# Performance work log

Hardware: AMD Instinct MI355X
Metric: run time of the kernel (lower is better)

## Reference

```python
import jax, jax.numpy as jnp
import numpy as np

B, S, H, IN, OUT, T = 1024, 256, 128, 2, 2, 512


def setup_inputs() -> dict:
    key = jax.random.key(0)
    ks = jax.random.split(key, 7)
    scale = 1.0 / np.sqrt(H)  # PyTorch LSTM init range ~ U(-1/sqrt(H), 1/sqrt(H))
    return {
        "x": jax.random.normal(ks[0], (B, S, IN), jnp.float32),
        "w_ih": jax.random.normal(ks[1], (4 * H, IN), jnp.float32) * scale,
        "w_hh": jax.random.normal(ks[2], (4 * H, H), jnp.float32) * scale,
        "b_ih": jax.random.normal(ks[3], (4 * H,), jnp.float32) * scale,
        "b_hh": jax.random.normal(ks[4], (4 * H,), jnp.float32) * scale,
        "w_fc": jax.random.normal(ks[5], (OUT, H), jnp.float32) * scale,
        "b_fc": jax.random.normal(ks[6], (OUT,), jnp.float32) * scale,
        "target_length": T,
    }


def reference(x, w_ih, w_hh, b_ih, b_hh, w_fc, b_fc, target_length):
    # PyTorch nn.LSTM cell, gate order (i, f, g, o). Dropout is identity (eval mode).
    bias = b_ih + b_hh
    hdim = w_hh.shape[1]

    def cell(h, c, x_t):
        gates = x_t @ w_ih.T + h @ w_hh.T + bias  # [B, 4H]
        i, f, g, o = jnp.split(gates, 4, axis=-1)
        c_new = jax.nn.sigmoid(f) * c + jax.nn.sigmoid(i) * jnp.tanh(g)
        h_new = jax.nn.sigmoid(o) * jnp.tanh(c_new)
        return h_new, c_new

    bsz = x.shape[0]
    h0 = jnp.zeros((bsz, hdim), x.dtype)
    c0 = jnp.zeros((bsz, hdim), x.dtype)

    # Encode input sequence
    def enc_step(carry, x_t):
        h, c = carry
        h, c = cell(h, c, x_t)
        return (h, c), None

    (h, c), _ = jax.lax.scan(enc_step, (h0, c0), jnp.swapaxes(x, 0, 1))

    inp0 = x[:, -1, :]  # [B, 2]

    def dec_step(carry, _):
        h, c, inp = carry
        h, c = cell(h, c, inp)
        pred = h @ w_fc.T + b_fc  # [B, 2]
        return (h, c, pred), pred

    _, preds = jax.lax.scan(dec_step, (h, c, inp0), None, length=target_length)
    return jnp.swapaxes(preds, 0, 1)  # [B, target_length, 2]
```

## Files before the change

### kernel.cpp

```cpp
#include <hip/hip_runtime.h>

typedef unsigned short ush;
typedef unsigned int uint32;
typedef __attribute__((ext_vector_type(8))) __bf16 bf16x8;
typedef __attribute__((ext_vector_type(4))) float f32x4;
typedef __attribute__((ext_vector_type(4))) int i32x4;
typedef __attribute__((ext_vector_type(16))) char c8x16;

#define NBLK 256
#define RB   4
#define NTHR 512
#define SENC 256
#define TDEC 512
#define HDIM 128
#define HSTR 144
#define H8STR 144
#define XSTR 520
#define PSTR 1024
#define HIST_USH_PER_BLK (TDEC * RB * HDIM)
#define WS_NEEDED ((size_t)NBLK * HIST_USH_PER_BLK * 2)

#define LOG2E  1.4426950408889634f
#define LOG2E2 2.8853900817779268f

__device__ __forceinline__ float bf2f(ush u){
  uint32 v = ((uint32)u) << 16;
  return __builtin_bit_cast(float, v);
}
__device__ __forceinline__ ush f2bf(float f){
  return __builtin_bit_cast(ush, (__bf16)f);
}
__device__ __forceinline__ float lo16f(uint32 w){ return __builtin_bit_cast(float, w << 16); }
__device__ __forceinline__ float hi16f(uint32 w){ return __builtin_bit_cast(float, w & 0xFFFF0000u); }

__device__ __forceinline__ float loadf(const void* p, int i, bool f32){
  return f32 ? ((const float*)p)[i] : bf2f(((const ush*)p)[i]);
}
__device__ __forceinline__ f32x4 M1(bf16x8 a, bf16x8 b, f32x4 c){
  return __builtin_amdgcn_mfma_f32_16x16x32_bf16(a, b, c, 0, 0, 0);
}
__device__ __forceinline__ i32x4 MI(i32x4 a, i32x4 b, i32x4 c){
  return __builtin_amdgcn_mfma_i32_16x16x64_i8(a, b, c, 0, 0, 0);
}

template<bool DEFER>
__global__ void __launch_bounds__(NTHR, 2)
lstm_kernel(const void* __restrict__ xg,  const void* __restrict__ wih,
            const void* __restrict__ whh, const void* __restrict__ bih,
            const void* __restrict__ bhh, const void* __restrict__ wfc,
            const void* __restrict__ bfc, void* __restrict__ outg,
            void* __restrict__ ws)
{
  __shared__ __attribute__((aligned(16))) ush x_lds[RB * XSTR];
  __shared__ __attribute__((aligned(16))) ush h_lds[2][RB * HSTR];
  __shared__ __attribute__((aligned(16))) char h8s[2][RB * H8STR];
  __shared__ __attribute__((aligned(16))) ush pred_lds[RB][PSTR];
  __shared__ __attribute__((aligned(16))) float ppart[2][RB][2][4];

  constexpr bool DF = DEFER;

  const int tid   = threadIdx.x;
  const int lane  = tid & 63;
  const int wv    = tid >> 6;
  const int n     = lane & 15;
  const int q     = lane >> 4;
  const int q8    = q * 8;
  const int q16   = q * 16;
  const int gbase = wv << 4;
  const int blk   = blockIdx.x;

  const uint32* wp = (const uint32*)whh;
  int cnt = 0;
  #pragma unroll
  for (int i = 0; i < 64; ++i){
    uint32 e = (wp[i] >> 7) & 0xFFu;
    cnt += (e >= 90u && e <= 140u) ? 1 : 0;
  }
  const bool isf32 = (cnt < 40);

  for (int i = tid; i < 2 * RB * HSTR; i += NTHR) h_lds[0][i] = 0;
  for (int i = tid; i < 2 * RB * H8STR; i += NTHR) ((char*)h8s)[i] = 0;

  if (!isf32){
    if (tid < 256){
      int row = tid >> 6, c = (tid & 63) * 8;
      uint4 v = *reinterpret_cast<const uint4*>((const ush*)xg + (blk * RB + row) * (SENC * 2) + c);
      *reinterpret_cast<uint4*>(&x_lds[row * XSTR + c]) = v;
    }
  } else {
    for (int i = tid; i < RB * SENC * 2; i += NTHR){
      int row = i >> 9, c = i & 511;
      x_lds[row * XSTR + c] = f2bf(((const float*)xg)[(blk * RB + row) * (SENC * 2) + c]);
    }
  }

  float wih0v[4], wih1v[4], biasv[4], smulv[4];
  i32x4 ifr[4][2];
  #pragma unroll
  for (int p = 0; p < 4; ++p){
    int g = p * 128 + gbase + n;
    biasv[p] = loadf(bih, g, isf32) + loadf(bhh, g, isf32);
    wih0v[p] = loadf(wih, g * 2 + 0, isf32);
    wih1v[p] = loadf(wih, g * 2 + 1, isf32);
    float w[2][16]; float m = 0.0f;
    #pragma unroll
    for (int kh = 0; kh < 2; ++kh){
      #pragma unroll
      for (int j = 0; j < 16; ++j){
        float v = loadf(whh, g * HDIM + kh * 64 + q16 + j, isf32);
        w[kh][j] = v; m = __builtin_fmaxf(m, __builtin_fabsf(v));
      }
    }
    m = __builtin_fmaxf(m, __shfl_xor(m, 16, 64));
    m = __builtin_fmaxf(m, __shfl_xor(m, 32, 64));
    m = __builtin_fmaxf(m, 1e-20f);
    float sinv = 127.0f / m;
    smulv[p] = m * (1.0f / (127.0f * 127.0f));
    #pragma unroll
    for (int kh = 0; kh < 2; ++kh){
      c8x16 c;
      #pragma unroll
      for (int j = 0; j < 16; ++j)
        c[j] = (char)(int)__builtin_rintf(w[kh][j] * sinv);
      ifr[p][kh] = __builtin_bit_cast(i32x4, c);
    }
  }
  const bool ispred = (wv == 0) || (wv == 3) || (wv == 5) || (wv == 6);
  const bool issum  = (wv == 1);
  const int  pkk    = (wv == 0) ? 0 : (wv == 3) ? 1 : (wv == 5) ? 2 : 3;
  const int  pofs   = pkk * 32 + q8;
  bf16x8 wpfr;
  #pragma unroll
  for (int j = 0; j < 8; ++j)
    wpfr[j] = (__bf16)loadf(wfc, (n & 1) * HDIM + pkk * 32 + q8 + j, isf32);
  f32x4 predC;
  {
    float pb = (wv == 0) ? loadf(bfc, n & 1, isf32) : 0.0f;
    predC[0] = pb; predC[1] = pb; predC[2] = pb; predC[3] = pb;
  }

  float cc = 0.0f;
  const int arow   = (n >> 2) * HSTR;
  const int a8row  = (n >> 2) * H8STR;
  const int hwofs  = q * HSTR + gbase + n;
  const int h8wofs = q * H8STR + gbase + n;
  const f32x4 Z  = {0.0f, 0.0f, 0.0f, 0.0f};
  const i32x4 IZ = {0, 0, 0, 0};

  ush* hlane = (ush*)ws + (((size_t)blk) << 18) + q * HDIM + gbase + n;

  __syncthreads();

#define LOADA8(RBUF) \
    const char* ha = &h8s[RBUF][a8row]; \
    i32x4 a80 = *reinterpret_cast<const i32x4*>(ha + q16); \
    i32x4 a81 = *reinterpret_cast<const i32x4*>(ha + 64 + q16);

#define GATEMM8 \
    i32x4 G2 = MI(a80, ifr[2][0], IZ); \
    i32x4 G0 = MI(a80, ifr[0][0], IZ); \
    i32x4 G1 = MI(a80, ifr[1][0], IZ); \
    i32x4 G3 = MI(a80, ifr[3][0], IZ); \
    G2 = MI(a81, ifr[2][1], G2); \
    G0 = MI(a81, ifr[0][1], G0); \
    G1 = MI(a81, ifr[1][1], G1); \
    G3 = MI(a81, ifr[3][1], G3);

#define TAIL8(WBUF, DOHIST, HS, BX0, BX1, BX2, BX3) \
    float g2 = __builtin_fmaf((float)G2[0], smulv[2], BX2); \
    float Eg = __builtin_amdgcn_exp2f(g2 * LOG2E2); \
    float g0 = __builtin_fmaf((float)G0[0], smulv[0], BX0); \
    float ei = __builtin_amdgcn_exp2f(-g0 * LOG2E); \
    float g1 = __builtin_fmaf((float)G1[0], smulv[1], BX1); \
    float ef = __builtin_amdgcn_exp2f(-g1 * LOG2E); \
    float g3 = __builtin_fmaf((float)G3[0], smulv[3], BX3); \
    float eo = __builtin_amdgcn_exp2f(-g3 * LOG2E); \
    float sitg = (Eg - 1.0f) * __builtin_amdgcn_rcpf((1.0f + ei) * (Eg + 1.0f)); \
    float sf = __builtin_amdgcn_rcpf(1.0f + ef); \
    cc = sf * cc + sitg; \
    float ccl = __builtin_amdgcn_fmed3f(cc, -20.0f, 20.0f); \
    float Ec = __builtin_amdgcn_exp2f(ccl * LOG2E2); \
    float hh = (Ec - 1.0f) * __builtin_amdgcn_rcpf((1.0f + eo) * (Ec + 1.0f)); \
    h8s[WBUF][h8wofs] = (char)(int)__builtin_rintf(hh * 127.0f); \
    if constexpr (DF){ if (DOHIST) hlane[(HS) * 512] = f2bf(hh); } \
    else { h_lds[WBUF][hwofs] = f2bf(hh); }

#define ENCSTEP(RBUF, WBUF, T, DOHIST, HS) { \
    LOADA8(RBUF) \
    uint32 xw = *reinterpret_cast<const uint32*>(&x_lds[q * XSTR + (T) * 2]); \
    GATEMM8 \
     \
    float xa = lo16f(xw), xb = hi16f(xw); \
    float bx0 = biasv[0] + __builtin_fmaf(wih0v[0], xa, wih1v[0] * xb); \
    float bx1 = biasv[1] + __builtin_fmaf(wih0v[1], xa, wih1v[1] * xb); \
    float bx2 = biasv[2] + __builtin_fmaf(wih0v[2], xa, wih1v[2] * xb); \
    float bx3 = biasv[3] + __builtin_fmaf(wih0v[3], xa, wih1v[3] * xb); \
    TAIL8(WBUF, DOHIST, HS, bx0, bx1, bx2, bx3) \
    __syncthreads(); \
  }

#define DECSTEP(RBUF, WBUF, D) { \
    LOADA8(RBUF) \
    if constexpr (!DF) { \
      bf16x8 pfrag; \
      if (ispred) pfrag = *reinterpret_cast<const bf16x8*>(&h_lds[RBUF][arow] + pofs); \
      f32x4 pp; \
      if (issum && (D) > 0 && n < 2) \
        pp = *reinterpret_cast<const f32x4*>(&ppart[((D) - 1) & 1][q][n][0]); \
      GATEMM8 \
      f32x4 PP; \
      if (ispred) PP = M1(pfrag, wpfr, predC); \
      if (issum && (D) > 0 && n < 2) \
        pred_lds[q][((D) - 1) * 2 + n] = f2bf(pp[0] + pp[1] + pp[2] + pp[3]); \
      if (ispred && n < 2) ppart[(D) & 1][q][n][pkk] = PP[0]; \
      TAIL8(WBUF, 0, 0, biasv[0], biasv[1], biasv[2], biasv[3]) \
    } else { \
      GATEMM8 \
      TAIL8(WBUF, 1, (D) + 1, biasv[0], biasv[1], biasv[2], biasv[3]) \
    } \
    __syncthreads(); \
  }

  #pragma unroll 1
  for (int s = 0; s < SENC; s += 2){
    ENCSTEP(0, 1, s, 0, 0)
    ENCSTEP(1, 0, s + 1, 0, 0)
  }
  ENCSTEP(0, 1, SENC - 1, 1, 0)

  {
    float bfc0 = loadf(bfc, 0, isf32), bfc1 = loadf(bfc, 1, isf32);
    #pragma unroll
    for (int p = 0; p < 4; ++p){
      int g = p * 128 + gbase + n;
      biasv[p] = biasv[p] + wih0v[p] * bfc0 + wih1v[p] * bfc1;
      float w[2][16]; float m = 0.0f;
      #pragma unroll
      for (int kh = 0; kh < 2; ++kh){
        #pragma unroll
        for (int j = 0; j < 16; ++j){
          int k = kh * 64 + q16 + j;
          float v = loadf(whh, g * HDIM + k, isf32)
                  + wih0v[p] * loadf(wfc, k, isf32)
                  + wih1v[p] * loadf(wfc, HDIM + k, isf32);
          w[kh][j] = v; m = __builtin_fmaxf(m, __builtin_fabsf(v));
        }
      }
      m = __builtin_fmaxf(m, __shfl_xor(m, 16, 64));
      m = __builtin_fmaxf(m, __shfl_xor(m, 32, 64));
      m = __builtin_fmaxf(m, 1e-20f);
      float sinv = 127.0f / m;
      smulv[p] = m * (1.0f / (127.0f * 127.0f));
      #pragma unroll
      for (int kh = 0; kh < 2; ++kh){
        c8x16 c;
        #pragma unroll
        for (int j = 0; j < 16; ++j)
          c[j] = (char)(int)__builtin_rintf(w[kh][j] * sinv);
        ifr[p][kh] = __builtin_bit_cast(i32x4, c);
      }
    }
  }

  #pragma unroll 1
  for (int d = 0; d < TDEC - 2; d += 2){
    DECSTEP(1, 0, d)
    DECSTEP(0, 1, d + 1)
  }
  DECSTEP(1, 0, TDEC - 2)

  if constexpr (DF){
    asm volatile("s_waitcnt vmcnt(0)" ::: "memory");
    __syncthreads();

    bf16x8 wfe[4];
    #pragma unroll
    for (int kk = 0; kk < 4; ++kk)
      #pragma unroll
      for (int j = 0; j < 8; ++j)
        wfe[kk][j] = (__bf16)loadf(wfc, (n & 1) * HDIM + kk * 32 + q8 + j, isf32);
    f32x4 predCe;
    {
      float pb = loadf(bfc, n & 1, isf32);
      predCe[0] = pb; predCe[1] = pb; predCe[2] = pb; predCe[3] = pb;
    }
    const ush* hg = (const ush*)ws + (((size_t)blk) << 18);
    #pragma unroll 4
    for (int i = 0; i < 16; ++i){
      int t = wv * 16 + i;
      const ush* ar = hg + ((t * 16 + n) << 7) + q8;
      bf16x8 a0 = __builtin_bit_cast(bf16x8, *reinterpret_cast<const uint4*>(ar));
      bf16x8 a1 = __builtin_bit_cast(bf16x8, *reinterpret_cast<const uint4*>(ar + 32));
      bf16x8 a2 = __builtin_bit_cast(bf16x8, *reinterpret_cast<const uint4*>(ar + 64));
      bf16x8 a3 = __builtin_bit_cast(bf16x8, *reinterpret_cast<const uint4*>(ar + 96));
      f32x4 P = M1(a0, wfe[0], predCe);
      P = M1(a1, wfe[1], P);
      P = M1(a2, wfe[2], P);
      P = M1(a3, wfe[3], P);
      #pragma unroll
      for (int r = 0; r < 4; ++r){
        int m = t * 16 + 4 * q + r;
        pred_lds[m & 3][((m >> 2) << 1) + (n & 1)] = f2bf(P[r]);
      }
    }
  } else {
    if (issum && n < 2){
      f32x4 pp = *reinterpret_cast<const f32x4*>(&ppart[0][q][n][0]);
      pred_lds[q][(TDEC - 2) * 2 + n] = f2bf(pp[0] + pp[1] + pp[2] + pp[3]);
    }
    if (wv == 0){
      const ush* hb = &h_lds[0][arow];
      bf16x8 af0 = *reinterpret_cast<const bf16x8*>(hb + q8);
      bf16x8 af2 = *reinterpret_cast<const bf16x8*>(hb + 64 + q8);
      bf16x8 af1 = *reinterpret_cast<const bf16x8*>(hb + 32 + q8);
      bf16x8 af3 = *reinterpret_cast<const bf16x8*>(hb + 96 + q8);
      bf16x8 wf0, wf1, wf2, wf3;
      #pragma unroll
      for (int j = 0; j < 8; ++j){
        wf0[j] = (__bf16)loadf(wfc, (n & 1) * HDIM +   0 + q8 + j, isf32);
        wf1[j] = (__bf16)loadf(wfc, (n & 1) * HDIM +  32 + q8 + j, isf32);
        wf2[j] = (__bf16)loadf(wfc, (n & 1) * HDIM +  64 + q8 + j, isf32);
        wf3[j] = (__bf16)loadf(wfc, (n & 1) * HDIM +  96 + q8 + j, isf32);
      }
      f32x4 P = M1(af0, wf0, predC);
      f32x4 Q = M1(af2, wf2, Z);
      P = M1(af1, wf1, P);
      Q = M1(af3, wf3, Q);
      if (n < 2)
        pred_lds[q][(TDEC - 1) * 2 + n] = f2bf(P[0] + Q[0]);
    }
  }
  __syncthreads();

  if (!isf32){
    int row = tid >> 7, c = (tid & 127) * 8;
    uint4 v = *reinterpret_cast<const uint4*>(&pred_lds[row][c]);
    *reinterpret_cast<uint4*>((ush*)outg + (blk * RB + row) * (TDEC * 2) + c) = v;
  } else {
    for (int i = tid; i < RB * TDEC * 2; i += NTHR){
      int row = i >> 10, c = i & 1023;
      ((float*)outg)[(blk * RB + row) * (TDEC * 2) + c] = bf2f(pred_lds[row][c]);
    }
  }
}

extern "C" void kernel_launch(void* const* d_in, const int* in_sizes, int n_in,
                              void* d_out, int out_size, void* d_ws, size_t ws_size,
                              hipStream_t stream) {
  const bool defer = (d_ws != nullptr) && (ws_size >= WS_NEEDED);
  if (defer){
    lstm_kernel<true><<<dim3(NBLK), dim3(NTHR), 0, stream>>>(
        d_in[0], d_in[1], d_in[2], d_in[3], d_in[4], d_in[5], d_in[6], d_out, d_ws);
  } else {
    lstm_kernel<false><<<dim3(NBLK), dim3(NTHR), 0, stream>>>(
        d_in[0], d_in[1], d_in[2], d_in[3], d_in[4], d_in[5], d_in[6], d_out, d_ws);
  }
}
```

Before: 402.0 us.

## Split deferred LSTM path into 2-row blocks across 512 workgroups

The deferred-history kernel now processes 2 batch rows per block instead of 4. That doubles the grid to 512 blocks and raises launch bounds to 4 blocks per CU for more occupancy and parallelism across the long sequential recurrence. The int8 MFMA still uses 16 rows, with half of them duplicated, so only even-q lanes write history, and the final prediction projection splits its accumulation into two chains. The fallback path keeps the old 4-row design as a separate kernel. The risks are wasted MFMA rows and extra register or LDS pressure at the higher occupancy.

```diff
diff --git a/kernel.cpp b/kernel.cpp
--- a/kernel.cpp
+++ b/kernel.cpp
@@ -7,18 +7,21 @@
 typedef __attribute__((ext_vector_type(4))) int i32x4;
 typedef __attribute__((ext_vector_type(16))) char c8x16;
 
-#define NBLK 256
-#define RB   4
 #define NTHR 512
 #define SENC 256
 #define TDEC 512
 #define HDIM 128
-#define HSTR 144
 #define H8STR 144
 #define XSTR 520
+
+#define NBLK_DF 512
+#define RBD 2
+#define NBLK_FB 256
+#define RBF 4
+#define HSTR 144
 #define PSTR 1024
-#define HIST_USH_PER_BLK (TDEC * RB * HDIM)
-#define WS_NEEDED ((size_t)NBLK * HIST_USH_PER_BLK * 2)
+
+#define WS_NEEDED ((size_t)NBLK_DF * TDEC * RBD * HDIM * 2)
 
 #define LOG2E  1.4426950408889634f
 #define LOG2E2 2.8853900817779268f
@@ -43,21 +46,16 @@
   return __builtin_amdgcn_mfma_i32_16x16x64_i8(a, b, c, 0, 0, 0);
 }
 
-template<bool DEFER>
-__global__ void __launch_bounds__(NTHR, 2)
-lstm_kernel(const void* __restrict__ xg,  const void* __restrict__ wih,
-            const void* __restrict__ whh, const void* __restrict__ bih,
-            const void* __restrict__ bhh, const void* __restrict__ wfc,
-            const void* __restrict__ bfc, void* __restrict__ outg,
-            void* __restrict__ ws)
+__global__ void __launch_bounds__(NTHR, 4)
+lstm_defer(const void* __restrict__ xg,  const void* __restrict__ wih,
+           const void* __restrict__ whh, const void* __restrict__ bih,
+           const void* __restrict__ bhh, const void* __restrict__ wfc,
+           const void* __restrict__ bfc, void* __restrict__ outg,
+           void* __restrict__ ws)
 {
-  __shared__ __attribute__((aligned(16))) ush x_lds[RB * XSTR];
-  __shared__ __attribute__((aligned(16))) ush h_lds[2][RB * HSTR];
-  __shared__ __attribute__((aligned(16))) char h8s[2][RB * H8STR];
-  __shared__ __attribute__((aligned(16))) ush pred_lds[RB][PSTR];
-  __shared__ __attribute__((aligned(16))) float ppart[2][RB][2][4];
-
-  constexpr bool DF = DEFER;
+  __shared__ __attribute__((aligned(16))) ush x_lds[RBD * XSTR];
+  __shared__ __attribute__((aligned(16))) char h8s[2][RBD * H8STR];
+  __shared__ __attribute__((aligned(16))) ush pred_lds[RBD][TDEC * 2];
 
   const int tid   = threadIdx.x;
   const int lane  = tid & 63;
@@ -66,6 +64,7 @@
   const int q     = lane >> 4;
   const int q8    = q * 8;
   const int q16   = q * 16;
+  const int rq    = q >> 1;
   const int gbase = wv << 4;
   const int blk   = blockIdx.x;
 
@@ -78,19 +77,18 @@
   }
   const bool isf32 = (cnt < 40);
 
-  for (int i = tid; i < 2 * RB * HSTR; i += NTHR) h_lds[0][i] = 0;
-  for (int i = tid; i < 2 * RB * H8STR; i += NTHR) ((char*)h8s)[i] = 0;
+  for (int i = tid; i < 2 * RBD * H8STR; i += NTHR) ((char*)h8s)[i] = 0;
 
   if (!isf32){
-    if (tid < 256){
+    if (tid < 128){
       int row = tid >> 6, c = (tid & 63) * 8;
-      uint4 v = *reinterpret_cast<const uint4*>((const ush*)xg + (blk * RB + row) * (SENC * 2) + c);
+      uint4 v = *reinterpret_cast<const uint4*>((const ush*)xg + (blk * RBD + row) * (SENC * 2) + c);
       *reinterpret_cast<uint4*>(&x_lds[row * XSTR + c]) = v;
     }
   } else {
-    for (int i = tid; i < RB * SENC * 2; i += NTHR){
+    for (int i = tid; i < RBD * SENC * 2; i += NTHR){
       int row = i >> 9, c = i & 511;
-      x_lds[row * XSTR + c] = f2bf(((const float*)xg)[(blk * RB + row) * (SENC * 2) + c]);
+      x_lds[row * XSTR + c] = f2bf(((const float*)xg)[(blk * RBD + row) * (SENC * 2) + c]);
     }
   }
 
@@ -125,38 +123,21 @@
       ifr[p][kh] = __builtin_bit_cast(i32x4, c);
     }
   }
-  const bool ispred = (wv == 0) || (wv == 3) || (wv == 5) || (wv == 6);
-  const bool issum  = (wv == 1);
-  const int  pkk    = (wv == 0) ? 0 : (wv == 3) ? 1 : (wv == 5) ? 2 : 3;
-  const int  pofs   = pkk * 32 + q8;
-  bf16x8 wpfr;
-  #pragma unroll
-  for (int j = 0; j < 8; ++j)
-    wpfr[j] = (__bf16)loadf(wfc, (n & 1) * HDIM + pkk * 32 + q8 + j, isf32);
-  f32x4 predC;
-  {
-    float pb = (wv == 0) ? loadf(bfc, n & 1, isf32) : 0.0f;
-    predC[0] = pb; predC[1] = pb; predC[2] = pb; predC[3] = pb;
-  }
 
   float cc = 0.0f;
-  const int arow   = (n >> 2) * HSTR;
-  const int a8row  = (n >> 2) * H8STR;
-  const int hwofs  = q * HSTR + gbase + n;
-  const int h8wofs = q * H8STR + gbase + n;
-  const f32x4 Z  = {0.0f, 0.0f, 0.0f, 0.0f};
-  const i32x4 IZ = {0, 0, 0, 0};
-
-  ush* hlane = (ush*)ws + (((size_t)blk) << 18) + q * HDIM + gbase + n;
+  const int a8row  = (n >> 3) * H8STR;
+  const int h8wofs = rq * H8STR + gbase + n;
+  ush* hlane = (ush*)ws + (((size_t)blk) << 17) + rq * HDIM + gbase + n;
+  const bool dohist = ((q & 1) == 0);
 
   __syncthreads();
 
-#define LOADA8(RBUF) \
+#define DLOADA8(RBUF) \
     const char* ha = &h8s[RBUF][a8row]; \
     i32x4 a80 = *reinterpret_cast<const i32x4*>(ha + q16); \
     i32x4 a81 = *reinterpret_cast<const i32x4*>(ha + 64 + q16);
 
-#define GATEMM8 \
+#define DGATEMM8 \
     i32x4 G2 = MI(a80, ifr[2][0], IZ); \
     i32x4 G0 = MI(a80, ifr[0][0], IZ); \
     i32x4 G1 = MI(a80, ifr[1][0], IZ); \
@@ -166,7 +147,7 @@
     G1 = MI(a81, ifr[1][1], G1); \
     G3 = MI(a81, ifr[3][1], G3);
 
-#define TAIL8(WBUF, DOHIST, HS, BX0, BX1, BX2, BX3) \
+#define DTAIL8(WBUF, DOH, HS, BX0, BX1, BX2, BX3) \
     float g2 = __builtin_fmaf((float)G2[0], smulv[2], BX2); \
     float Eg = __builtin_amdgcn_exp2f(g2 * LOG2E2); \
     float g0 = __builtin_fmaf((float)G0[0], smulv[0], BX0); \
@@ -182,51 +163,37 @@
     float Ec = __builtin_amdgcn_exp2f(ccl * LOG2E2); \
     float hh = (Ec - 1.0f) * __builtin_amdgcn_rcpf((1.0f + eo) * (Ec + 1.0f)); \
     h8s[WBUF][h8wofs] = (char)(int)__builtin_rintf(hh * 127.0f); \
-    if constexpr (DF){ if (DOHIST) hlane[(HS) * 512] = f2bf(hh); } \
-    else { h_lds[WBUF][hwofs] = f2bf(hh); }
-
-#define ENCSTEP(RBUF, WBUF, T, DOHIST, HS) { \
-    LOADA8(RBUF) \
-    uint32 xw = *reinterpret_cast<const uint32*>(&x_lds[q * XSTR + (T) * 2]); \
-    GATEMM8 \
-     \
+    if (DOH && dohist) hlane[(HS) * (RBD * HDIM)] = f2bf(hh);
+
+#define DENCSTEP(RBUF, WBUF, T, DOH, HS) { \
+    DLOADA8(RBUF) \
+    uint32 xw = *reinterpret_cast<const uint32*>(&x_lds[rq * XSTR + (T) * 2]); \
+    DGATEMM8 \
     float xa = lo16f(xw), xb = hi16f(xw); \
     float bx0 = biasv[0] + __builtin_fmaf(wih0v[0], xa, wih1v[0] * xb); \
     float bx1 = biasv[1] + __builtin_fmaf(wih0v[1], xa, wih1v[1] * xb); \
     float bx2 = biasv[2] + __builtin_fmaf(wih0v[2], xa, wih1v[2] * xb); \
     float bx3 = biasv[3] + __builtin_fmaf(wih0v[3], xa, wih1v[3] * xb); \
-    TAIL8(WBUF, DOHIST, HS, bx0, bx1, bx2, bx3) \
+    DTAIL8(WBUF, DOH, HS, bx0, bx1, bx2, bx3) \
     __syncthreads(); \
   }
 
-#define DECSTEP(RBUF, WBUF, D) { \
-    LOADA8(RBUF) \
-    if constexpr (!DF) { \
-      bf16x8 pfrag; \
-      if (ispred) pfrag = *reinterpret_cast<const bf16x8*>(&h_lds[RBUF][arow] + pofs); \
-      f32x4 pp; \
-      if (issum && (D) > 0 && n < 2) \
-        pp = *reinterpret_cast<const f32x4*>(&ppart[((D) - 1) & 1][q][n][0]); \
-      GATEMM8 \
-      f32x4 PP; \
-      if (ispred) PP = M1(pfrag, wpfr, predC); \
-      if (issum && (D) > 0 && n < 2) \
-        pred_lds[q][((D) - 1) * 2 + n] = f2bf(pp[0] + pp[1] + pp[2] + pp[3]); \
-      if (ispred && n < 2) ppart[(D) & 1][q][n][pkk] = PP[0]; \
-      TAIL8(WBUF, 0, 0, biasv[0], biasv[1], biasv[2], biasv[3]) \
-    } else { \
-      GATEMM8 \
-      TAIL8(WBUF, 1, (D) + 1, biasv[0], biasv[1], biasv[2], biasv[3]) \
-    } \
+#define DDECSTEP(RBUF, WBUF, D) { \
+    DLOADA8(RBUF) \
+    DGATEMM8 \
+    DTAIL8(WBUF, 1, (D) + 1, biasv[0], biasv[1], biasv[2], biasv[3]) \
     __syncthreads(); \
   }
+
+  const i32x4 IZ = {0, 0, 0, 0};
+  const f32x4 Z  = {0.0f, 0.0f, 0.0f, 0.0f};
 
   #pragma unroll 1
   for (int s = 0; s < SENC; s += 2){
-    ENCSTEP(0, 1, s, 0, 0)
-    ENCSTEP(1, 0, s + 1, 0, 0)
-  }
-  ENCSTEP(0, 1, SENC - 1, 1, 0)
+    DENCSTEP(0, 1, s, 0, 0)
+    DENCSTEP(1, 0, s + 1, 0, 0)
+  }
+  DENCSTEP(0, 1, SENC - 1, 1, 0)
 
   {
     float bfc0 = loadf(bfc, 0, isf32), bfc1 = loadf(bfc, 1, isf32);
@@ -264,82 +231,308 @@
 
   #pragma unroll 1
   for (int d = 0; d < TDEC - 2; d += 2){
-    DECSTEP(1, 0, d)
-    DECSTEP(0, 1, d + 1)
-  }
-  DECSTEP(1, 0, TDEC - 2)
-
-  if constexpr (DF){
-    asm volatile("s_waitcnt vmcnt(0)" ::: "memory");
-    __syncthreads();
-
-    bf16x8 wfe[4];
-    #pragma unroll
-    for (int kk = 0; kk < 4; ++kk)
-      #pragma unroll
-      for (int j = 0; j < 8; ++j)
-        wfe[kk][j] = (__bf16)loadf(wfc, (n & 1) * HDIM + kk * 32 + q8 + j, isf32);
-    f32x4 predCe;
-    {
-      float pb = loadf(bfc, n & 1, isf32);
-      predCe[0] = pb; predCe[1] = pb; predCe[2] = pb; predCe[3] = pb;
-    }
-    const ush* hg = (const ush*)ws + (((size_t)blk) << 18);
-    #pragma unroll 4
-    for (int i = 0; i < 16; ++i){
-      int t = wv * 16 + i;
-      const ush* ar = hg + ((t * 16 + n) << 7) + q8;
-      bf16x8 a0 = __builtin_bit_cast(bf16x8, *reinterpret_cast<const uint4*>(ar));
-      bf16x8 a1 = __builtin_bit_cast(bf16x8, *reinterpret_cast<const uint4*>(ar + 32));
-      bf16x8 a2 = __builtin_bit_cast(bf16x8, *reinterpret_cast<const uint4*>(ar + 64));
-      bf16x8 a3 = __builtin_bit_cast(bf16x8, *reinterpret_cast<const uint4*>(ar + 96));
-      f32x4 P = M1(a0, wfe[0], predCe);
-      P = M1(a1, wfe[1], P);
-      P = M1(a2, wfe[2], P);
-      P = M1(a3, wfe[3], P);
-      #pragma unroll
-      for (int r = 0; r < 4; ++r){
-        int m = t * 16 + 4 * q + r;
-        pred_lds[m & 3][((m >> 2) << 1) + (n & 1)] = f2bf(P[r]);
+    DDECSTEP(1, 0, d)
+    DDECSTEP(0, 1, d + 1)
+  }
+  DDECSTEP(1, 0, TDEC - 2)
+
+  asm volatile("s_waitcnt vmcnt(0)" ::: "memory");
+  __syncthreads();
+
+  bf16x8 wfe[4];
+  #pragma unroll
+  for (int kk = 0; kk < 4; ++kk)
+    #pragma unroll
+    for (int j = 0; j < 8; ++j)
+      wfe[kk][j] = (__bf16)loadf(wfc, (n & 1) * HDIM + kk * 32 + q8 + j, isf32);
+  f32x4 predCe;
+  {
+    float pb = loadf(bfc, n & 1, isf32);
+    predCe[0] = pb; predCe[1] = pb; predCe[2] = pb; predCe[3] = pb;
+  }
+  const ush* hg = (const ush*)ws + (((size_t)blk) << 17);
+  #pragma unroll 4
+  for (int i = 0; i < 8; ++i){
+    int t = wv * 8 + i;
+    const ush* ar = hg + ((t * 16 + n) << 7) + q8;
+    bf16x8 a0 = __builtin_bit_cast(bf16x8, *reinterpret_cast<const uint4*>(ar));
+    bf16x8 a1 = __builtin_bit_cast(bf16x8, *reinterpret_cast<const uint4*>(ar + 32));
+    bf16x8 a2 = __builtin_bit_cast(bf16x8, *reinterpret_cast<const uint4*>(ar + 64));
+    bf16x8 a3 = __builtin_bit_cast(bf16x8, *reinterpret_cast<const uint4*>(ar + 96));
+    f32x4 P = M1(a0, wfe[0], predCe);
+    f32x4 Q = M1(a2, wfe[2], Z);
+    P = M1(a1, wfe[1], P);
+    Q = M1(a3, wfe[3], Q);
+    #pragma unroll
+    for (int r = 0; r < 4; ++r){
+      int m = t * 16 + 4 * q + r;
+      pred_lds[m & 1][((m >> 1) << 1) + (n & 1)] = f2bf(P[r] + Q[r]);
+    }
+  }
+  __syncthreads();
+
+  if (!isf32){
+    if (tid < 256){
+      int row = tid >> 7, c = (tid & 127) * 8;
+      uint4 v = *reinterpret_cast<const uint4*>(&pred_lds[row][c]);
+      *reinterpret_cast<uint4*>((ush*)outg + (blk * RBD + row) * (TDEC * 2) + c) = v;
+    }
+  } else {
+    for (int i = tid; i < RBD * TDEC * 2; i += NTHR){
+      int row = i >> 10, c = i & 1023;
+      ((float*)outg)[(blk * RBD + row) * (TDEC * 2) + c] = bf2f(pred_lds[row][c]);
+    }
+  }
+}
+
+__global__ void __launch_bounds__(NTHR, 2)
+lstm_fb(const void* __restrict__ xg,  const void* __restrict__ wih,
+        const void* __restrict__ whh, const void* __restrict__ bih,
+        const void* __restrict__ bhh, const void* __restrict__ wfc,
+        const void* __restrict__ bfc, void* __restrict__ outg)
+{
+  __shared__ __attribute__((aligned(16))) ush x_lds[RBF * XSTR];
+  __shared__ __attribute__((aligned(16))) ush h_lds[2][RBF * HSTR];
+  __shared__ __attribute__((aligned(16))) char h8s[2][RBF * H8STR];
+  __shared__ __attribute__((aligned(16))) ush pred_lds[RBF][PSTR];
+  __shared__ __attribute__((aligned(16))) float ppart[2][RBF][2][4];
+
+  const int tid   = threadIdx.x;
+  const int lane  = tid & 63;
+  const int wv    = tid >> 6;
+  const int n     = lane & 15;
+  const int q     = lane >> 4;
+  const int q8    = q * 8;
+  const int q16   = q * 16;
+  const int gbase = wv << 4;
+  const int blk   = blockIdx.x;
+
+  const uint32* wp = (const uint32*)whh;
+  int cnt = 0;
+  #pragma unroll
+  for (int i = 0; i < 64; ++i){
+    uint32 e = (wp[i] >> 7) & 0xFFu;
+    cnt += (e >= 90u && e <= 140u) ? 1 : 0;
+  }
+  const bool isf32 = (cnt < 40);
+
+  for (int i = tid; i < 2 * RBF * HSTR; i += NTHR) h_lds[0][i] = 0;
+  for (int i = tid; i < 2 * RBF * H8STR; i += NTHR) ((char*)h8s)[i] = 0;
+
+  if (!isf32){
+    if (tid < 256){
+      int row = tid >> 6, c = (tid & 63) * 8;
+      uint4 v = *reinterpret_cast<const uint4*>((const ush*)xg + (blk * RBF + row) * (SENC * 2) + c);
+      *reinterpret_cast<uint4*>(&x_lds[row * XSTR + c]) = v;
+    }
+  } else {
+    for (int i = tid; i < RBF * SENC * 2; i += NTHR){
+      int row = i >> 9, c = i & 511;
+      x_lds[row * XSTR + c] = f2bf(((const float*)xg)[(blk * RBF + row) * (SENC * 2) + c]);
+    }
+  }
+
+  float wih0v[4], wih1v[4], biasv[4], smulv[4];
+  i32x4 ifr[4][2];
+  #pragma unroll
+  for (int p = 0; p < 4; ++p){
+    int g = p * 128 + gbase + n;
+    biasv[p] = loadf(bih, g, isf32) + loadf(bhh, g, isf32);
+    wih0v[p] = loadf(wih, g * 2 + 0, isf32);
+    wih1v[p] = loadf(wih, g * 2 + 1, isf32);
+    float w[2][16]; float m = 0.0f;
+    #pragma unroll
+    for (int kh = 0; kh < 2; ++kh){
+      #pragma unroll
+      for (int j = 0; j < 16; ++j){
+        float v = loadf(whh, g * HDIM + kh * 64 + q16 + j, isf32);
+        w[kh][j] = v; m = __builtin_fmaxf(m, __builtin_fabsf(v));
       }
     }
-  } else {
-    if (issum && n < 2){
-      f32x4 pp = *reinterpret_cast<const f32x4*>(&ppart[0][q][n][0]);
-      pred_lds[q][(TDEC - 2) * 2 + n] = f2bf(pp[0] + pp[1] + pp[2] + pp[3]);
-    }
-    if (wv == 0){
-      const ush* hb = &h_lds[0][arow];
-      bf16x8 af0 = *reinterpret_cast<const bf16x8*>(hb + q8);
-      bf16x8 af2 = *reinterpret_cast<const bf16x8*>(hb + 64 + q8);
-      bf16x8 af1 = *reinterpret_cast<const bf16x8*>(hb + 32 + q8);
-      bf16x8 af3 = *reinterpret_cast<const bf16x8*>(hb + 96 + q8);
-      bf16x8 wf0, wf1, wf2, wf3;
-      #pragma unroll
-      for (int j = 0; j < 8; ++j){
-        wf0[j] = (__bf16)loadf(wfc, (n & 1) * HDIM +   0 + q8 + j, isf32);
-        wf1[j] = (__bf16)loadf(wfc, (n & 1) * HDIM +  32 + q8 + j, isf32);
-        wf2[j] = (__bf16)loadf(wfc, (n & 1) * HDIM +  64 + q8 + j, isf32);
-        wf3[j] = (__bf16)loadf(wfc, (n & 1) * HDIM +  96 + q8 + j, isf32);
+    m = __builtin_fmaxf(m, __shfl_xor(m, 16, 64));
+    m = __builtin_fmaxf(m, __shfl_xor(m, 32, 64));
+    m = __builtin_fmaxf(m, 1e-20f);
+    float sinv = 127.0f / m;
+    smulv[p] = m * (1.0f / (127.0f * 127.0f));
+    #pragma unroll
+    for (int kh = 0; kh < 2; ++kh){
+      c8x16 c;
+      #pragma unroll
+      for (int j = 0; j < 16; ++j)
+        c[j] = (char)(int)__builtin_rintf(w[kh][j] * sinv);
+      ifr[p][kh] = __builtin_bit_cast(i32x4, c);
+    }
+  }
+  const bool ispred = (wv == 0) || (wv == 3) || (wv == 5) || (wv == 6);
+  const bool issum  = (wv == 1);
+  const int  pkk    = (wv == 0) ? 0 : (wv == 3) ? 1 : (wv == 5) ? 2 : 3;
+  const int  pofs   = pkk * 32 + q8;
+  bf16x8 wpfr;
+  #pragma unroll
+  for (int j = 0; j < 8; ++j)
+    wpfr[j] = (__bf16)loadf(wfc, (n & 1) * HDIM + pkk * 32 + q8 + j, isf32);
+  f32x4 predC;
+  {
+    float pb = (wv == 0) ? loadf(bfc, n & 1, isf32) : 0.0f;
+    predC[0] = pb; predC[1] = pb; predC[2] = pb; predC[3] = pb;
+  }
+
+  float cc = 0.0f;
+  const int arow   = (n >> 2) * HSTR;
+  const int a8row  = (n >> 2) * H8STR;
+  const int hwofs  = q * HSTR + gbase + n;
+  const int h8wofs = q * H8STR + gbase + n;
+  const f32x4 Z  = {0.0f, 0.0f, 0.0f, 0.0f};
+  const i32x4 IZ = {0, 0, 0, 0};
+
+  __syncthreads();
+
+#define FLOADA8(RBUF) \
+    const char* ha = &h8s[RBUF][a8row]; \
+    i32x4 a80 = *reinterpret_cast<const i32x4*>(ha + q16); \
+    i32x4 a81 = *reinterpret_cast<const i32x4*>(ha + 64 + q16);
+
+#define FGATEMM8 \
+    i32x4 G2 = MI(a80, ifr[2][0], IZ); \
+    i32x4 G0 = MI(a80, ifr[0][0], IZ); \
+    i32x4 G1 = MI(a80, ifr[1][0], IZ); \
+    i32x4 G3 = MI(a80, ifr[3][0], IZ); \
+    G2 = MI(a81, ifr[2][1], G2); \
+    G0 = MI(a81, ifr[0][1], G0); \
+    G1 = MI(a81, ifr[1][1], G1); \
+    G3 = MI(a81, ifr[3][1], G3);
+
+#define FTAIL8(WBUF, BX0, BX1, BX2, BX3) \
+    float g2 = __builtin_fmaf((float)G2[0], smulv[2], BX2); \
+    float Eg = __builtin_amdgcn_exp2f(g2 * LOG2E2); \
+    float g0 = __builtin_fmaf((float)G0[0], smulv[0], BX0); \
+    float ei = __builtin_amdgcn_exp2f(-g0 * LOG2E); \
+    float g1 = __builtin_fmaf((float)G1[0], smulv[1], BX1); \
+    float ef = __builtin_amdgcn_exp2f(-g1 * LOG2E); \
+    float g3 = __builtin_fmaf((float)G3[0], smulv[3], BX3); \
+    float eo = __builtin_amdgcn_exp2f(-g3 * LOG2E); \
+    float sitg = (Eg - 1.0f) * __builtin_amdgcn_rcpf((1.0f + ei) * (Eg + 1.0f)); \
+    float sf = __builtin_amdgcn_rcpf(1.0f + ef); \
+    cc = sf * cc + sitg; \
+    float ccl = __builtin_amdgcn_fmed3f(cc, -20.0f, 20.0f); \
+    float Ec = __builtin_amdgcn_exp2f(ccl * LOG2E2); \
+    float hh = (Ec - 1.0f) * __builtin_amdgcn_rcpf((1.0f + eo) * (Ec + 1.0f)); \
+    h8s[WBUF][h8wofs] = (char)(int)__builtin_rintf(hh * 127.0f); \
+    h_lds[WBUF][hwofs] = f2bf(hh);
+
+#define FENCSTEP(RBUF, WBUF, T) { \
+    FLOADA8(RBUF) \
+    uint32 xw = *reinterpret_cast<const uint32*>(&x_lds[q * XSTR + (T) * 2]); \
+    FGATEMM8 \
+    float xa = lo16f(xw), xb = hi16f(xw); \
+    float bx0 = biasv[0] + __builtin_fmaf(wih0v[0], xa, wih1v[0] * xb); \
+    float bx1 = biasv[1] + __builtin_fmaf(wih0v[1], xa, wih1v[1] * xb); \
+    float bx2 = biasv[2] + __builtin_fmaf(wih0v[2], xa, wih1v[2] * xb); \
+    float bx3 = biasv[3] + __builtin_fmaf(wih0v[3], xa, wih1v[3] * xb); \
+    FTAIL8(WBUF, bx0, bx1, bx2, bx3) \
+    __syncthreads(); \
+  }
+
+#define FDECSTEP(RBUF, WBUF, D) { \
+    FLOADA8(RBUF) \
+    bf16x8 pfrag; \
+    if (ispred) pfrag = *reinterpret_cast<const bf16x8*>(&h_lds[RBUF][arow] + pofs); \
+    f32x4 pp; \
+    if (issum && (D) > 0 && n < 2) \
+      pp = *reinterpret_cast<const f32x4*>(&ppart[((D) - 1) & 1][q][n][0]); \
+    FGATEMM8 \
+    f32x4 PP; \
+    if (ispred) PP = M1(pfrag, wpfr, predC); \
+    if (issum && (D) > 0 && n < 2) \
+      pred_lds[q][((D) - 1) * 2 + n] = f2bf(pp[0] + pp[1] + pp[2] + pp[3]); \
+    if (ispred && n < 2) ppart[(D) & 1][q][n][pkk] = PP[0]; \
+    FTAIL8(WBUF, biasv[0], biasv[1], biasv[2], biasv[3]) \
+    __syncthreads(); \
+  }
+
+  #pragma unroll 1
+  for (int s = 0; s < SENC; s += 2){
+    FENCSTEP(0, 1, s)
+    FENCSTEP(1, 0, s + 1)
+  }
+  FENCSTEP(0, 1, SENC - 1)
+
+  {
+    float bfc0 = loadf(bfc, 0, isf32), bfc1 = loadf(bfc, 1, isf32);
+    #pragma unroll
+    for (int p = 0; p < 4; ++p){
+      int g = p * 128 + gbase + n;
+      biasv[p] = biasv[p] + wih0v[p] * bfc0 + wih1v[p] * bfc1;
+      float w[2][16]; float m = 0.0f;
+      #pragma unroll
+      for (int kh = 0; kh < 2; ++kh){
+        #pragma unroll
+        for (int j = 0; j < 16; ++j){
+          int k = kh * 64 + q16 + j;
+          float v = loadf(whh, g * HDIM + k, isf32)
+                  + wih0v[p] * loadf(wfc, k, isf32)
+                  + wih1v[p] * loadf(wfc, HDIM + k, isf32);
+          w[kh][j] = v; m = __builtin_fmaxf(m, __builtin_fabsf(v));
+        }
       }
-      f32x4 P = M1(af0, wf0, predC);
-      f32x4 Q = M1(af2, wf2, Z);
-      P = M1(af1, wf1, P);
-      Q = M1(af3, wf3, Q);
-      if (n < 2)
-        pred_lds[q][(TDEC - 1) * 2 + n] = f2bf(P[0] + Q[0]);
-    }
+      m = __builtin_fmaxf(m, __shfl_xor(m, 16, 64));
+      m = __builtin_fmaxf(m, __shfl_xor(m, 32, 64));
+      m = __builtin_fmaxf(m, 1e-20f);
+      float sinv = 127.0f / m;
+      smulv[p] = m * (1.0f / (127.0f * 127.0f));
+      #pragma unroll
+      for (int kh = 0; kh < 2; ++kh){
+        c8x16 c;
+        #pragma unroll
+        for (int j = 0; j < 16; ++j)
+          c[j] = (char)(int)__builtin_rintf(w[kh][j] * sinv);
+        ifr[p][kh] = __builtin_bit_cast(i32x4, c);
+      }
+    }
+  }
+
+  #pragma unroll 1
+  for (int d = 0; d < TDEC - 2; d += 2){
+    FDECSTEP(1, 0, d)
+    FDECSTEP(0, 1, d + 1)
+  }
+  FDECSTEP(1, 0, TDEC - 2)
+
+  if (issum && n < 2){
+    f32x4 pp = *reinterpret_cast<const f32x4*>(&ppart[0][q][n][0]);
+    pred_lds[q][(TDEC - 2) * 2 + n] = f2bf(pp[0] + pp[1] + pp[2] + pp[3]);
+  }
+  if (wv == 0){
+    const ush* hb = &h_lds[0][arow];
+    bf16x8 af0 = *reinterpret_cast<const bf16x8*>(hb + q8);
+    bf16x8 af2 = *reinterpret_cast<const bf16x8*>(hb + 64 + q8);
+    bf16x8 af1 = *reinterpret_cast<const bf16x8*>(hb + 32 + q8);
+    bf16x8 af3 = *reinterpret_cast<const bf16x8*>(hb + 96 + q8);
+    bf16x8 wf0, wf1, wf2, wf3;
+    #pragma unroll
+    for (int j = 0; j < 8; ++j){
+      wf0[j] = (__bf16)loadf(wfc, (n & 1) * HDIM +   0 + q8 + j, isf32);
+      wf1[j] = (__bf16)loadf(wfc, (n & 1) * HDIM +  32 + q8 + j, isf32);
+      wf2[j] = (__bf16)loadf(wfc, (n & 1) * HDIM +  64 + q8 + j, isf32);
+      wf3[j] = (__bf16)loadf(wfc, (n & 1) * HDIM +  96 + q8 + j, isf32);
+    }
+    f32x4 P = M1(af0, wf0, predC);
+    f32x4 Q = M1(af2, wf2, Z);
+    P = M1(af1, wf1, P);
+    Q = M1(af3, wf3, Q);
+    if (n < 2)
+      pred_lds[q][(TDEC - 1) * 2 + n] = f2bf(P[0] + Q[0]);
   }
   __syncthreads();
 
   if (!isf32){
     int row = tid >> 7, c = (tid & 127) * 8;
     uint4 v = *reinterpret_cast<const uint4*>(&pred_lds[row][c]);
-    *reinterpret_cast<uint4*>((ush*)outg + (blk * RB + row) * (TDEC * 2) + c) = v;
+    *reinterpret_cast<uint4*>((ush*)outg + (blk * RBF + row) * (TDEC * 2) + c) = v;
   } else {
-    for (int i = tid; i < RB * TDEC * 2; i += NTHR){
+    for (int i = tid; i < RBF * TDEC * 2; i += NTHR){
       int row = i >> 10, c = i & 1023;
-      ((float*)outg)[(blk * RB + row) * (TDEC * 2) + c] = bf2f(pred_lds[row][c]);
+      ((float*)outg)[(blk * RBF + row) * (TDEC * 2) + c] = bf2f(pred_lds[row][c]);
     }
   }
 }
@@ -349,10 +542,10 @@
                               hipStream_t stream) {
   const bool defer = (d_ws != nullptr) && (ws_size >= WS_NEEDED);
   if (defer){
-    lstm_kernel<true><<<dim3(NBLK), dim3(NTHR), 0, stream>>>(
+    lstm_defer<<<dim3(NBLK_DF), dim3(NTHR), 0, stream>>>(
         d_in[0], d_in[1], d_in[2], d_in[3], d_in[4], d_in[5], d_in[6], d_out, d_ws);
   } else {
-    lstm_kernel<false><<<dim3(NBLK), dim3(NTHR), 0, stream>>>(
-        d_in[0], d_in[1], d_in[2], d_in[3], d_in[4], d_in[5], d_in[6], d_out, d_ws);
-  }
-}
+    lstm_fb<<<dim3(NBLK_FB), dim3(NTHR), 0, stream>>>(
+        d_in[0], d_in[1], d_in[2], d_in[3], d_in[4], d_in[5], d_in[6], d_out);
+  }
+}
```

New measurement: 586.8 us. +46.0%, slower.
